# Optimization experiments

Hardware: AMD Instinct MI355X
Metric: run time of the kernel (lower is better)

## Reference

```python
import jax, jax.numpy as jnp
import numpy as np

NC, NP_, E = 100000, 50000, 500000
DC, DP = 256, 128
HID, OUT = 64, 64
H1, H2 = 2, 1
SLOPE = 0.2


def setup_inputs() -> dict:
    key = jax.random.key(0)
    ks = jax.random.split(key, 32)
    d = {}
    d['x_customer'] = jax.random.normal(ks[0], (NC, DC), jnp.float32)
    d['x_product'] = jax.random.normal(ks[1], (NP_, DP), jnp.float32)
    d['edge_src'] = jax.random.randint(ks[2], (E,), 0, NC, jnp.int32)
    d['edge_dst'] = jax.random.randint(ks[3], (E,), 0, NP_, jnp.int32)
    s = 0.1
    # layer1, edge type (customer, buys, product): src=customer, dst=product
    d['w1b_src'] = jax.random.normal(ks[4], (DC, H1 * HID)) * s
    d['w1b_dst'] = jax.random.normal(ks[5], (DP, H1 * HID)) * s
    d['a1b_src'] = jax.random.normal(ks[6], (H1, HID)) * s
    d['a1b_dst'] = jax.random.normal(ks[7], (H1, HID)) * s
    d['b1b'] = jnp.zeros((H1 * HID,), jnp.float32)
    # layer1, edge type (product, rev_buys, customer): src=product, dst=customer
    d['w1r_src'] = jax.random.normal(ks[8], (DP, H1 * HID)) * s
    d['w1r_dst'] = jax.random.normal(ks[9], (DC, H1 * HID)) * s
    d['a1r_src'] = jax.random.normal(ks[10], (H1, HID)) * s
    d['a1r_dst'] = jax.random.normal(ks[11], (H1, HID)) * s
    d['b1r'] = jnp.zeros((H1 * HID,), jnp.float32)
    # layer2 (input dim = H1*HID = 128 for both node types), heads=1
    d['w2b_src'] = jax.random.normal(ks[12], (H1 * HID, H2 * OUT)) * s
    d['w2b_dst'] = jax.random.normal(ks[13], (H1 * HID, H2 * OUT)) * s
    d['a2b_src'] = jax.random.normal(ks[14], (H2, OUT)) * s
    d['a2b_dst'] = jax.random.normal(ks[15], (H2, OUT)) * s
    d['b2b'] = jnp.zeros((H2 * OUT,), jnp.float32)
    d['w2r_src'] = jax.random.normal(ks[16], (H1 * HID, H2 * OUT)) * s
    d['w2r_dst'] = jax.random.normal(ks[17], (H1 * HID, H2 * OUT)) * s
    d['a2r_src'] = jax.random.normal(ks[18], (H2, OUT)) * s
    d['a2r_dst'] = jax.random.normal(ks[19], (H2, OUT)) * s
    d['b2r'] = jnp.zeros((H2 * OUT,), jnp.float32)
    return d


def _gat_conv(h_src, h_dst, e_src, e_dst, att_src, att_dst, bias, n_dst):
    # h_src: [Ns,H,C] projected source feats; h_dst: [Nd,H,C]
    a_s = (h_src * att_src).sum(-1)  # [Ns,H]
    a_d = (h_dst * att_dst).sum(-1)  # [Nd,H]
    alpha = jax.nn.leaky_relu(a_s[e_src] + a_d[e_dst], negative_slope=SLOPE)  # [E,H]
    m = jax.lax.stop_gradient(jax.ops.segment_max(alpha, e_dst, num_segments=n_dst))
    ex = jnp.exp(alpha - m[e_dst])
    den = jax.ops.segment_sum(ex, e_dst, num_segments=n_dst)
    w = ex / (den[e_dst] + 1e-16)  # segment softmax over incoming edges
    msg = h_src[e_src] * w[..., None]  # [E,H,C]
    out = jax.ops.segment_sum(msg, e_dst, num_segments=n_dst)  # [Nd,H,C]
    return out.reshape(n_dst, -1) + bias


def reference(x_customer, x_product, edge_src, edge_dst,
              w1b_src, w1b_dst, a1b_src, a1b_dst, b1b,
              w1r_src, w1r_dst, a1r_src, a1r_dst, b1r,
              w2b_src, w2b_dst, a2b_src, a2b_dst, b2b,
              w2r_src, w2r_dst, a2r_src, a2r_dst, b2r):
    # ---- layer 1 (heads=2, concat) ----
    hs = (x_customer @ w1b_src).reshape(NC, H1, HID)
    hd = (x_product @ w1b_dst).reshape(NP_, H1, HID)
    p1 = _gat_conv(hs, hd, edge_src, edge_dst, a1b_src, a1b_dst, b1b, NP_)
    hs = (x_product @ w1r_src).reshape(NP_, H1, HID)
    hd = (x_customer @ w1r_dst).reshape(NC, H1, HID)
    c1 = _gat_conv(hs, hd, edge_dst, edge_src, a1r_src, a1r_dst, b1r, NC)
    c1 = jax.nn.relu(c1)
    p1 = jax.nn.relu(p1)
    # ---- layer 2 (heads=1) ----
    hs = (c1 @ w2b_src).reshape(NC, H2, OUT)
    hd = (p1 @ w2b_dst).reshape(NP_, H2, OUT)
    p2 = _gat_conv(hs, hd, edge_src, edge_dst, a2b_src, a2b_dst, b2b, NP_)
    hs = (p1 @ w2r_src).reshape(NP_, H2, OUT)
    hd = (c1 @ w2r_dst).reshape(NC, H2, OUT)
    c2 = _gat_conv(hs, hd, edge_dst, edge_src, a2r_src, a2r_dst, b2r, NC)
    return c2, p2
```

## Files before the change

### kernel.cpp

```cpp
#include <hip/hip_runtime.h>
#include <hip/hip_bf16.h>

typedef __bf16 bf16_t;
typedef bf16_t bf16x2 __attribute__((ext_vector_type(2)));
typedef bf16_t bf16x4 __attribute__((ext_vector_type(4)));
typedef bf16_t bf16x8 __attribute__((ext_vector_type(8)));
typedef float f32x2 __attribute__((ext_vector_type(2)));
typedef float f32x4 __attribute__((ext_vector_type(4)));

static constexpr int NCn = 100000;
static constexpr int NPn = 50000;
static constexpr int NE  = 500000;

__device__ __forceinline__ float ldin(const void* p, size_t i, int fp32) {
    return fp32 ? ((const float*)p)[i] : (float)((const bf16_t*)p)[i];
}

__global__ __launch_bounds__(64) void detect_dtype(const void* x, int* flag) {
    const bf16_t* xb = (const bf16_t*)x;
    int lane = threadIdx.x;
    int bad = 0;
    for (int i = lane; i < 512; i += 64) {
        float v = (float)xb[i];
        if (!(v > -1e4f && v < 1e4f)) bad = 1;
    }
    unsigned long long m = __ballot(bad);
    if (lane == 0) flag[0] = (m != 0ull) ? 1 : 0;
}

__global__ __launch_bounds__(256) void zero_int(int* __restrict__ p, int n) {
    int i = blockIdx.x * 256 + threadIdx.x;
    if (i < n) p[i] = 0;
}
__global__ __launch_bounds__(256) void copy_int(const int* __restrict__ s,
                                                int* __restrict__ d, int n) {
    int i = blockIdx.x * 256 + threadIdx.x;
    if (i < n) d[i] = s[i];
}

__global__ __launch_bounds__(256) void prep_V(const int* __restrict__ flag,
                                              const void* w1bd, const void* a1bd,
                                              const void* w1rd, const void* a1rd,
                                              const void* w2bd, const void* a2bd,
                                              const void* w2rd, const void* a2rd,
                                              float* V1bd, float* V1rd,
                                              float* V2bd, float* V2rd) {
    int fp32 = flag[0];
    int t = threadIdx.x;
    for (int idx = t; idx < 256; idx += 256) {
        int k = idx >> 1, h = idx & 1;
        float s = 0.f;
        for (int c = 0; c < 64; ++c)
            s += ldin(w1bd, (size_t)k * 128 + h * 64 + c, fp32) * ldin(a1bd, h * 64 + c, fp32);
        V1bd[k * 2 + h] = s;
    }
    for (int idx = t; idx < 512; idx += 256) {
        int k = idx >> 1, h = idx & 1;
        float s = 0.f;
        for (int c = 0; c < 64; ++c)
            s += ldin(w1rd, (size_t)k * 128 + h * 64 + c, fp32) * ldin(a1rd, h * 64 + c, fp32);
        V1rd[k * 2 + h] = s;
    }
    for (int k = t; k < 128; k += 256) {
        float s = 0.f;
        for (int c = 0; c < 64; ++c)
            s += ldin(w2bd, (size_t)k * 64 + c, fp32) * ldin(a2bd, c, fp32);
        V2bd[k] = s;
    }
    for (int k = t; k < 128; k += 256) {
        float s = 0.f;
        for (int c = 0; c < 64; ++c)
            s += ldin(w2rd, (size_t)k * 64 + c, fp32) * ldin(a2rd, c, fp32);
        V2rd[k] = s;
    }
}

__global__ __launch_bounds__(256) void prep_w(const void* __restrict__ W,
                                              bf16_t* __restrict__ Wt,
                                              int N, int ks,
                                              const int* __restrict__ flag) {
    int fp32 = flag[0];
    int idx = blockIdx.x * 256 + threadIdx.x;
    int K = 1 << ks;
    int n = idx >> ks, k = idx & (K - 1);
    if (n < N) Wt[idx] = (bf16_t)ldin(W, (size_t)k * N + n, fp32);
}

template<int K>
__global__ __launch_bounds__(256) void cvt_rows(const void* __restrict__ X,
                                                bf16_t* __restrict__ Xb,
                                                const float* __restrict__ V,
                                                float* __restrict__ ad,
                                                int M, const int* __restrict__ flag) {
    constexpr int EPL = K / 64;
    int fp32 = flag[0];
    int wid = (blockIdx.x * 256 + threadIdx.x) >> 6;
    int lane = threadIdx.x & 63;
    if (wid >= M) return;
    size_t base = (size_t)wid * K + lane * EPL;
    float x[EPL];
    if constexpr (EPL == 4) {
        if (fp32) { f32x4 t = *(const f32x4*)((const float*)X + base);
#pragma unroll
            for (int j = 0; j < 4; ++j) x[j] = t[j];
        } else { bf16x4 t = *(const bf16x4*)((const bf16_t*)X + base);
#pragma unroll
            for (int j = 0; j < 4; ++j) x[j] = (float)t[j];
        }
        bf16x4 o;
#pragma unroll
        for (int j = 0; j < 4; ++j) o[j] = (bf16_t)x[j];
        *(bf16x4*)(Xb + base) = o;
    } else {
        if (fp32) { f32x2 t = *(const f32x2*)((const float*)X + base);
#pragma unroll
            for (int j = 0; j < 2; ++j) x[j] = t[j];
        } else { bf16x2 t = *(const bf16x2*)((const bf16_t*)X + base);
#pragma unroll
            for (int j = 0; j < 2; ++j) x[j] = (float)t[j];
        }
        bf16x2 o;
#pragma unroll
        for (int j = 0; j < 2; ++j) o[j] = (bf16_t)x[j];
        *(bf16x2*)(Xb + base) = o;
    }
    float a0 = 0.f, a1 = 0.f;
#pragma unroll
    for (int j = 0; j < EPL; ++j) {
        int k = lane * EPL + j;
        a0 += x[j] * V[k * 2];
        a1 += x[j] * V[k * 2 + 1];
    }
    for (int off = 32; off; off >>= 1) {
        a0 += __shfl_down(a0, off);
        a1 += __shfl_down(a1, off);
    }
    if (lane == 0) { ad[(size_t)wid * 2] = a0; ad[(size_t)wid * 2 + 1] = a1; }
}

__global__ __launch_bounds__(256) void hist_k(const int* __restrict__ dst,
                                              int* __restrict__ cnt, int E) {
    int e = blockIdx.x * 256 + threadIdx.x;
    if (e < E) atomicAdd(&cnt[dst[e]], 1);
}

__global__ __launch_bounds__(256) void scan_blocks(const int* __restrict__ cnt,
                                                   int* __restrict__ rs,
                                                   int* __restrict__ bsum, int N) {
    int t = threadIdx.x, b = blockIdx.x;
    int base = b * 1024 + t * 4;
    int c[4];
#pragma unroll
    for (int k = 0; k < 4; ++k) { int i = base + k; c[k] = (i < N) ? cnt[i] : 0; }
    int tsum = c[0] + c[1] + c[2] + c[3];
    __shared__ int sd[256];
    sd[t] = tsum;
    __syncthreads();
    for (int off = 1; off < 256; off <<= 1) {
        int x = (t >= off) ? sd[t - off] : 0;
        __syncthreads();
        sd[t] += x;
        __syncthreads();
    }
    int run = sd[t] - tsum;
#pragma unroll
    for (int k = 0; k < 4; ++k) { int i = base + k; if (i < N) rs[i] = run; run += c[k]; }
    if (t == 255) bsum[b] = sd[255];
}

__global__ __launch_bounds__(128) void scan_bsum(int* bsum, int nb) {
    int t = threadIdx.x;
    __shared__ int sd[128];
    int v = (t < nb) ? bsum[t] : 0;
    sd[t] = v;
    __syncthreads();
    for (int off = 1; off < 128; off <<= 1) {
        int x = (t >= off) ? sd[t - off] : 0;
        __syncthreads();
        sd[t] += x;
        __syncthreads();
    }
    if (t < nb) bsum[t] = sd[t] - v;
}

__global__ __launch_bounds__(256) void scan_add(int* __restrict__ rs,
                                                const int* __restrict__ bsum,
                                                int N, int E) {
    int i = blockIdx.x * 256 + threadIdx.x;
    if (i < N) rs[i] += bsum[i >> 10];
    if (i == 0) rs[N] = E;
}

__global__ __launch_bounds__(256) void scatter_k(const int* __restrict__ dst,
                                                 const int* __restrict__ nbr,
                                                 int* __restrict__ cur,
                                                 int* __restrict__ srcs,
                                                 int* __restrict__ dsts, int E) {
    int e = blockIdx.x * 256 + threadIdx.x;
    if (e >= E) return;
    int d = dst[e];
    int pos = atomicAdd(&cur[d], 1);
    srcs[pos] = nbr[e];
    dsts[pos] = d;
}

template<int K>
__global__ __launch_bounds__(256) void gemm_nl(const bf16_t* __restrict__ A,
                                               const bf16_t* __restrict__ Wt,
                                               bf16_t* __restrict__ C,
                                               int M, int N) {
    const int w = threadIdx.x >> 6;
    const int lane = threadIdx.x & 63;
    const int lm = lane & 15;
    const int lq = lane >> 4;
    const int n0 = blockIdx.y * 64;
    const int r0 = blockIdx.x * 128 + w * 32;
    int ra0 = r0 + lm;       if (ra0 > M - 1) ra0 = M - 1;
    int ra1 = r0 + 16 + lm;  if (ra1 > M - 1) ra1 = M - 1;
    const bf16_t* A0 = A + (size_t)ra0 * K + lq * 8;
    const bf16_t* A1 = A + (size_t)ra1 * K + lq * 8;
    const bf16_t* B0 = Wt + (size_t)(n0 + lm) * K + lq * 8;
    f32x4 acc[2][4] = {};
#pragma unroll
    for (int kt = 0; kt < K / 32; ++kt) {
        bf16x8 a0 = *(const bf16x8*)(A0 + kt * 32);
        bf16x8 a1 = *(const bf16x8*)(A1 + kt * 32);
#pragma unroll
        for (int nt = 0; nt < 4; ++nt) {
            bf16x8 b = *(const bf16x8*)(B0 + (size_t)nt * 16 * K + kt * 32);
            acc[0][nt] = __builtin_amdgcn_mfma_f32_16x16x32_bf16(a0, b, acc[0][nt], 0, 0, 0);
            acc[1][nt] = __builtin_amdgcn_mfma_f32_16x16x32_bf16(a1, b, acc[1][nt], 0, 0, 0);
        }
    }
#pragma unroll
    for (int rt = 0; rt < 2; ++rt) {
        const int crow0 = r0 + rt * 16 + lq * 4;
#pragma unroll
        for (int nt = 0; nt < 4; ++nt) {
            int col = n0 + nt * 16 + lm;
#pragma unroll
            for (int i = 0; i < 4; ++i) {
                int r = crow0 + i;
                if (r < M) C[(size_t)r * N + col] = (bf16_t)acc[rt][nt][i];
            }
        }
    }
}

__global__ __launch_bounds__(256) void att_dot(const bf16_t* __restrict__ Hb,
                                               const void* __restrict__ att,
                                               float* __restrict__ out,
                                               int Nn, int HD, int H,
                                               const int* __restrict__ flag) {
    int fp32 = flag[0];
    int wid = (blockIdx.x * 256 + threadIdx.x) >> 6;
    int lane = threadIdx.x & 63;
    if (wid >= Nn) return;
    const bf16_t* hp = Hb + (size_t)wid * HD;
    float p0 = (float)hp[lane] * ldin(att, lane, fp32);
    float p1 = 0.f;
    if (HD > 64) p1 = (float)hp[64 + lane] * ldin(att, 64 + lane, fp32);
    for (int off = 32; off; off >>= 1) {
        p0 += __shfl_down(p0, off);
        p1 += __shfl_down(p1, off);
    }
    if (lane == 0) {
        out[(size_t)wid * H] = p0;
        if (H == 2) out[(size_t)wid * H + 1] = p1;
    }
}

template<int H>
__global__ __launch_bounds__(256) void edge_ex(const int* __restrict__ srcs,
                                               const int* __restrict__ dsts,
                                               const float* __restrict__ as_,
                                               const float* __restrict__ ad_,
                                               float* __restrict__ ex, int E) {
    int i = blockIdx.x * 256 + threadIdx.x;
    if (i >= E) return;
    int s = srcs[i], d = dsts[i];
    if constexpr (H == 2) {
        f32x2 a = *(const f32x2*)(as_ + 2 * (size_t)s);
        f32x2 b = *(const f32x2*)(ad_ + 2 * (size_t)d);
        float v0 = a[0] + b[0]; v0 = v0 > 0.f ? v0 : 0.2f * v0;
        float v1 = a[1] + b[1]; v1 = v1 > 0.f ? v1 : 0.2f * v1;
        f32x2 o;
        o[0] = __expf(fminf(v0, 60.f));
        o[1] = __expf(fminf(v1, 60.f));
        *(f32x2*)(ex + 2 * (size_t)i) = o;
    } else {
        float v = as_[s] + ad_[d];
        v = v > 0.f ? v : 0.2f * v;
        ex[i] = __expf(fminf(v, 60.f));
    }
}

template<int HD, int MODE>
__global__ __launch_bounds__(256) void aggregate(const int* __restrict__ rs,
                                                 const int* __restrict__ srcs,
                                                 const float* __restrict__ ex,
                                                 const bf16_t* __restrict__ Hm,
                                                 const void* __restrict__ bias,
                                                 void* __restrict__ outb, size_t obase,
                                                 const float* __restrict__ V2,
                                                 float* __restrict__ ad2,
                                                 int Nd, const int* __restrict__ flag) {
    constexpr int NH = HD / 64;
    int wid = (blockIdx.x * 256 + threadIdx.x) >> 6;
    int lane = threadIdx.x & 63;
    if (wid >= Nd) return;
    int start = rs[wid], end = rs[wid + 1];
    int fp32 = flag[0];
    const int hsel = lane >> 5;

    float den = 0.f, acc0 = 0.f, acc1 = 0.f;
#pragma unroll 4
    for (int j = start; j < end; ++j) {
        int s = srcs[j];
        if constexpr (NH == 2) {
            f32x2 e = *(const f32x2*)(ex + 2 * (size_t)j);
            float eh = hsel ? e[1] : e[0];
            den += eh;
            bf16x2 hv = *(const bf16x2*)(Hm + (size_t)s * 128 + 2 * lane);
            acc0 += (float)hv[0] * eh;
            acc1 += (float)hv[1] * eh;
        } else {
            float eh = ex[j];
            den += eh;
            acc0 += (float)Hm[(size_t)s * 64 + lane] * eh;
        }
    }
    float inv = 1.f / (den + 1e-16f);

    if constexpr (MODE == 0) {
        int c0 = 2 * lane;
        float o0 = fmaxf(acc0 * inv + ldin(bias, c0, fp32), 0.f);
        float o1 = fmaxf(acc1 * inv + ldin(bias, c0 + 1, fp32), 0.f);
        bf16x2 ov;
        ov[0] = (bf16_t)o0;
        ov[1] = (bf16_t)o1;
        *(bf16x2*)((bf16_t*)outb + (size_t)wid * 128 + c0) = ov;
        float pp = o0 * V2[c0] + o1 * V2[c0 + 1];
        for (int off = 32; off; off >>= 1) pp += __shfl_down(pp, off);
        if (lane == 0) ad2[wid] = pp;
    } else {
        float o = acc0 * inv + ldin(bias, lane, fp32);
        size_t oi = obase + (size_t)wid * 64 + lane;
        if (fp32) ((float*)outb)[oi] = o;
        else      ((bf16_t*)outb)[oi] = (bf16_t)o;
    }
}

extern "C" void kernel_launch(void* const* d_in, const int* in_sizes, int n_in,
                              void* d_out, int out_size, void* d_ws, size_t ws_size,
                              hipStream_t stream) {
    const void* xc = d_in[0];
    const void* xp = d_in[1];
    const int* esrc = (const int*)d_in[2];
    const int* edst = (const int*)d_in[3];
    const void* w1b_src = d_in[4];
    const void* w1b_dst = d_in[5];
    const void* a1b_src = d_in[6];
    const void* a1b_dst = d_in[7];
    const void* b1b     = d_in[8];
    const void* w1r_src = d_in[9];
    const void* w1r_dst = d_in[10];
    const void* a1r_src = d_in[11];
    const void* a1r_dst = d_in[12];
    const void* b1r     = d_in[13];
    const void* w2b_src = d_in[14];
    const void* w2b_dst = d_in[15];
    const void* a2b_src = d_in[16];
    const void* a2b_dst = d_in[17];
    const void* b2b     = d_in[18];
    const void* w2r_src = d_in[19];
    const void* w2r_dst = d_in[20];
    const void* a2r_src = d_in[21];
    const void* a2r_dst = d_in[22];
    const void* b2r     = d_in[23];

    char* p = (char*)d_ws;
    auto alloc = [&](size_t nbytes) {
        char* r = p;
        p += (nbytes + 255) & ~(size_t)255;
        return r;
    };
    int* flag   = (int*)alloc(256);
    float* V1bd = (float*)alloc(256 * 4);
    float* V1rd = (float*)alloc(512 * 4);
    float* V2bd = (float*)alloc(128 * 4);
    float* V2rd = (float*)alloc(128 * 4);
    bf16_t* Wt1b = (bf16_t*)alloc(128 * 256 * 2);
    bf16_t* Wt1r = (bf16_t*)alloc(128 * 128 * 2);
    bf16_t* Wt2b = (bf16_t*)alloc(64 * 128 * 2);
    bf16_t* Wt2r = (bf16_t*)alloc(64 * 128 * 2);
    float* as_s = (float*)alloc((size_t)NCn * 2 * 4);
    float* ad_b = (float*)alloc((size_t)NPn * 2 * 4);
    float* ad_r = (float*)alloc((size_t)NCn * 2 * 4);
    float* ad2_b = (float*)alloc((size_t)NPn * 4);
    float* ad2_r = (float*)alloc((size_t)NCn * 4);
    int* rsB    = (int*)alloc((size_t)(NPn + 1) * 4);
    int* rsR    = (int*)alloc((size_t)(NCn + 1) * 4);
    int* srcsB  = (int*)alloc((size_t)NE * 4);
    int* srcsR  = (int*)alloc((size_t)NE * 4);
    int* dstsB  = (int*)alloc((size_t)NE * 4);
    int* dstsR  = (int*)alloc((size_t)NE * 4);
    float* exB  = (float*)alloc((size_t)NE * 2 * 4);
    float* exR  = (float*)alloc((size_t)NE * 2 * 4);
    int* cntB   = (int*)alloc((size_t)NPn * 4);
    int* cntR   = (int*)alloc((size_t)NCn * 4);
    int* bsum   = (int*)alloc(128 * 4);
    bf16_t* xcb = (bf16_t*)alloc((size_t)NCn * 256 * 2);
    bf16_t* xpb = (bf16_t*)alloc((size_t)NPn * 128 * 2);
    bf16_t* Hc  = (bf16_t*)alloc((size_t)NCn * 128 * 2);
    bf16_t* Hp  = (bf16_t*)alloc((size_t)NPn * 128 * 2);
    bf16_t* c1  = (bf16_t*)alloc((size_t)NCn * 128 * 2);
    bf16_t* p1  = (bf16_t*)alloc((size_t)NPn * 128 * 2);
    bf16_t* Hc2 = (bf16_t*)alloc((size_t)NCn * 64 * 2);
    bf16_t* Hp2 = (bf16_t*)alloc((size_t)NPn * 64 * 2);

    const dim3 blk(256);
    const int gE = (NE + 255) / 256;
    const int sbP = (NPn + 1023) / 1024;
    const int sbR = (NCn + 1023) / 1024;
    const int gmC = (NCn + 127) / 128;
    const int gmP = (NPn + 127) / 128;
    const int gNP = (NPn + 255) / 256;
    const int gNC = (NCn + 255) / 256;

    detect_dtype<<<1, 64, 0, stream>>>(xc, flag);
    prep_V<<<1, 256, 0, stream>>>(flag, w1b_dst, a1b_dst, w1r_dst, a1r_dst,
                                  w2b_dst, a2b_dst, w2r_dst, a2r_dst,
                                  V1bd, V1rd, V2bd, V2rd);
    prep_w<<<128, blk, 0, stream>>>(w1b_src, Wt1b, 128, 8, flag);
    prep_w<<<64,  blk, 0, stream>>>(w1r_src, Wt1r, 128, 7, flag);
    prep_w<<<32,  blk, 0, stream>>>(w2b_src, Wt2b, 64, 7, flag);
    prep_w<<<32,  blk, 0, stream>>>(w2r_src, Wt2r, 64, 7, flag);

    zero_int<<<gNP, blk, 0, stream>>>(cntB, NPn);
    hist_k<<<gE, blk, 0, stream>>>(edst, cntB, NE);
    scan_blocks<<<sbP, blk, 0, stream>>>(cntB, rsB, bsum, NPn);
    scan_bsum<<<1, 128, 0, stream>>>(bsum, sbP);
    scan_add<<<gNP + 1, blk, 0, stream>>>(rsB, bsum, NPn, NE);
    copy_int<<<gNP, blk, 0, stream>>>(rsB, cntB, NPn);
    scatter_k<<<gE, blk, 0, stream>>>(edst, esrc, cntB, srcsB, dstsB, NE);

    zero_int<<<gNC, blk, 0, stream>>>(cntR, NCn);
    hist_k<<<gE, blk, 0, stream>>>(esrc, cntR, NE);
    scan_blocks<<<sbR, blk, 0, stream>>>(cntR, rsR, bsum, NCn);
    scan_bsum<<<1, 128, 0, stream>>>(bsum, sbR);
    scan_add<<<gNC + 1, blk, 0, stream>>>(rsR, bsum, NCn, NE);
    copy_int<<<gNC, blk, 0, stream>>>(rsR, cntR, NCn);
    scatter_k<<<gE, blk, 0, stream>>>(esrc, edst, cntR, srcsR, dstsR, NE);

    cvt_rows<256><<<(NCn + 3) / 4, blk, 0, stream>>>(xc, xcb, V1rd, ad_r, NCn, flag);
    cvt_rows<128><<<(NPn + 3) / 4, blk, 0, stream>>>(xp, xpb, V1bd, ad_b, NPn, flag);

    gemm_nl<256><<<dim3(gmC, 2), blk, 0, stream>>>(xcb, Wt1b, Hc, NCn, 128);
    gemm_nl<128><<<dim3(gmP, 2), blk, 0, stream>>>(xpb, Wt1r, Hp, NPn, 128);

    att_dot<<<(NCn + 3) / 4, blk, 0, stream>>>(Hc, a1b_src, as_s, NCn, 128, 2, flag);
    edge_ex<2><<<gE, blk, 0, stream>>>(srcsB, dstsB, as_s, ad_b, exB, NE);
    aggregate<128, 0><<<(NPn + 3) / 4, blk, 0, stream>>>(rsB, srcsB, exB, Hc, b1b, p1, 0, V2bd, ad2_b, NPn, flag);

    att_dot<<<(NPn + 3) / 4, blk, 0, stream>>>(Hp, a1r_src, as_s, NPn, 128, 2, flag);
    edge_ex<2><<<gE, blk, 0, stream>>>(srcsR, dstsR, as_s, ad_r, exR, NE);
    aggregate<128, 0><<<(NCn + 3) / 4, blk, 0, stream>>>(rsR, srcsR, exR, Hp, b1r, c1, 0, V2rd, ad2_r, NCn, flag);

    gemm_nl<128><<<dim3(gmC, 1), blk, 0, stream>>>(c1, Wt2b, Hc2, NCn, 64);
    gemm_nl<128><<<dim3(gmP, 1), blk, 0, stream>>>(p1, Wt2r, Hp2, NPn, 64);

    att_dot<<<(NCn + 3) / 4, blk, 0, stream>>>(Hc2, a2b_src, as_s, NCn, 64, 1, flag);
    edge_ex<1><<<gE, blk, 0, stream>>>(srcsB, dstsB, as_s, ad2_b, exB, NE);
    aggregate<64, 1><<<(NPn + 3) / 4, blk, 0, stream>>>(rsB, srcsB, exB, Hc2, b2b, d_out, (size_t)NCn * 64, nullptr, nullptr, NPn, flag);

    att_dot<<<(NPn + 3) / 4, blk, 0, stream>>>(Hp2, a2r_src, as_s, NPn, 64, 1, flag);
    edge_ex<1><<<gE, blk, 0, stream>>>(srcsR, dstsR, as_s, ad2_r, exR, NE);
    aggregate<64, 1><<<(NCn + 3) / 4, blk, 0, stream>>>(rsR, srcsR, exR, Hp2, b2r, d_out, 0, nullptr, nullptr, NCn, flag);
}
```

Baseline: 717.3 us.

## Fuse attention dot into GEMM epilogue and merge per-edge-type kernels

```diff
diff --git a/kernel.cpp b/kernel.cpp
--- a/kernel.cpp
+++ b/kernel.cpp
@@ -16,37 +16,27 @@
     return fp32 ? ((const float*)p)[i] : (float)((const bf16_t*)p)[i];
 }
 
-__global__ __launch_bounds__(64) void detect_dtype(const void* x, int* flag) {
-    const bf16_t* xb = (const bf16_t*)x;
-    int lane = threadIdx.x;
-    int bad = 0;
-    for (int i = lane; i < 512; i += 64) {
-        float v = (float)xb[i];
-        if (!(v > -1e4f && v < 1e4f)) bad = 1;
-    }
-    unsigned long long m = __ballot(bad);
-    if (lane == 0) flag[0] = (m != 0ull) ? 1 : 0;
-}
-
-__global__ __launch_bounds__(256) void zero_int(int* __restrict__ p, int n) {
-    int i = blockIdx.x * 256 + threadIdx.x;
-    if (i < n) p[i] = 0;
-}
-__global__ __launch_bounds__(256) void copy_int(const int* __restrict__ s,
-                                                int* __restrict__ d, int n) {
-    int i = blockIdx.x * 256 + threadIdx.x;
-    if (i < n) d[i] = s[i];
-}
-
-__global__ __launch_bounds__(256) void prep_V(const int* __restrict__ flag,
-                                              const void* w1bd, const void* a1bd,
-                                              const void* w1rd, const void* a1rd,
-                                              const void* w2bd, const void* a2bd,
-                                              const void* w2rd, const void* a2rd,
-                                              float* V1bd, float* V1rd,
-                                              float* V2bd, float* V2rd) {
-    int fp32 = flag[0];
+__global__ __launch_bounds__(256) void prep_meta(const void* x, int* flag,
+                                                 const void* w1bd, const void* a1bd,
+                                                 const void* w1rd, const void* a1rd,
+                                                 const void* w2bd, const void* a2bd,
+                                                 const void* w2rd, const void* a2rd,
+                                                 float* V1bd, float* V1rd,
+                                                 float* V2bd, float* V2rd) {
+    __shared__ int sflag;
     int t = threadIdx.x;
+    if (t < 64) {
+        const bf16_t* xb = (const bf16_t*)x;
+        int bad = 0;
+        for (int i = t; i < 512; i += 64) {
+            float v = (float)xb[i];
+            if (!(v > -1e4f && v < 1e4f)) bad = 1;
+        }
+        unsigned long long m = __ballot(bad);
+        if (t == 0) { sflag = (m != 0ull) ? 1 : 0; flag[0] = sflag; }
+    }
+    __syncthreads();
+    int fp32 = sflag;
     for (int idx = t; idx < 256; idx += 256) {
         int k = idx >> 1, h = idx & 1;
         float s = 0.f;
@@ -75,12 +65,19 @@
     }
 }
 
-__global__ __launch_bounds__(256) void prep_w(const void* __restrict__ W,
-                                              bf16_t* __restrict__ Wt,
-                                              int N, int ks,
-                                              const int* __restrict__ flag) {
+__global__ __launch_bounds__(256) void prep_w4(const void* __restrict__ w1b, bf16_t* __restrict__ Wt1b,
+                                               const void* __restrict__ w1r, bf16_t* __restrict__ Wt1r,
+                                               const void* __restrict__ w2b, bf16_t* __restrict__ Wt2b,
+                                               const void* __restrict__ w2r, bf16_t* __restrict__ Wt2r,
+                                               const int* __restrict__ flag) {
     int fp32 = flag[0];
-    int idx = blockIdx.x * 256 + threadIdx.x;
+    int b = blockIdx.x;
+    const void* W; bf16_t* Wt; int N, ks, base;
+    if (b < 128)      { W = w1b; Wt = Wt1b; N = 128; ks = 8; base = 0;   }
+    else if (b < 192) { W = w1r; Wt = Wt1r; N = 128; ks = 7; base = 128; }
+    else if (b < 224) { W = w2b; Wt = Wt2b; N = 64;  ks = 7; base = 192; }
+    else              { W = w2r; Wt = Wt2r; N = 64;  ks = 7; base = 224; }
+    int idx = (b - base) * 256 + threadIdx.x;
     int K = 1 << ks;
     int n = idx >> ks, k = idx & (K - 1);
     if (n < N) Wt[idx] = (bf16_t)ldin(W, (size_t)k * N + n, fp32);
@@ -138,10 +135,21 @@
     if (lane == 0) { ad[(size_t)wid * 2] = a0; ad[(size_t)wid * 2 + 1] = a1; }
 }
 
-__global__ __launch_bounds__(256) void hist_k(const int* __restrict__ dst,
-                                              int* __restrict__ cnt, int E) {
+__global__ __launch_bounds__(256) void zero2(int* __restrict__ a, int na,
+                                             int* __restrict__ b, int nb) {
+    int i = blockIdx.x * 256 + threadIdx.x;
+    if (i < na) a[i] = 0;
+    else if (i - na < nb) b[i - na] = 0;
+}
+
+__global__ __launch_bounds__(256) void hist2(const int* __restrict__ esrc,
+                                             const int* __restrict__ edst,
+                                             int* __restrict__ cntR,
+                                             int* __restrict__ cntB, int E) {
     int e = blockIdx.x * 256 + threadIdx.x;
-    if (e < E) atomicAdd(&cnt[dst[e]], 1);
+    if (e >= E) return;
+    atomicAdd(&cntB[edst[e]], 1);
+    atomicAdd(&cntR[esrc[e]], 1);
 }
 
 __global__ __launch_bounds__(256) void scan_blocks(const int* __restrict__ cnt,
@@ -168,7 +176,10 @@
     if (t == 255) bsum[b] = sd[255];
 }
 
-__global__ __launch_bounds__(128) void scan_bsum(int* bsum, int nb) {
+__global__ __launch_bounds__(128) void scan_bsum2(int* __restrict__ bsumB, int nbB,
+                                                  int* __restrict__ bsumR, int nbR) {
+    int* bsum = blockIdx.x ? bsumR : bsumB;
+    int nb = blockIdx.x ? nbR : nbB;
     int t = threadIdx.x;
     __shared__ int sd[128];
     int v = (t < nb) ? bsum[t] : 0;
@@ -183,32 +194,39 @@
     if (t < nb) bsum[t] = sd[t] - v;
 }
 
-__global__ __launch_bounds__(256) void scan_add(int* __restrict__ rs,
-                                                const int* __restrict__ bsum,
-                                                int N, int E) {
+__global__ __launch_bounds__(256) void scan_add2(int* __restrict__ rsB, const int* __restrict__ bsumB,
+                                                 int NB, int* __restrict__ cntB,
+                                                 int* __restrict__ rsR, const int* __restrict__ bsumR,
+                                                 int NR, int* __restrict__ cntR, int E) {
     int i = blockIdx.x * 256 + threadIdx.x;
-    if (i < N) rs[i] += bsum[i >> 10];
-    if (i == 0) rs[N] = E;
-}
-
-__global__ __launch_bounds__(256) void scatter_k(const int* __restrict__ dst,
-                                                 const int* __restrict__ nbr,
-                                                 int* __restrict__ cur,
-                                                 int* __restrict__ srcs,
-                                                 int* __restrict__ dsts, int E) {
+    if (i < NB) { int v = rsB[i] + bsumB[i >> 10]; rsB[i] = v; cntB[i] = v; }
+    if (i < NR) { int v = rsR[i] + bsumR[i >> 10]; rsR[i] = v; cntR[i] = v; }
+    if (i == 0) { rsB[NB] = E; rsR[NR] = E; }
+}
+
+__global__ __launch_bounds__(256) void scatter2(const int* __restrict__ esrc,
+                                                const int* __restrict__ edst,
+                                                int* __restrict__ curB, int* __restrict__ curR,
+                                                int* __restrict__ srcsB, int* __restrict__ dstsB,
+                                                int* __restrict__ srcsR, int* __restrict__ dstsR,
+                                                int E) {
     int e = blockIdx.x * 256 + threadIdx.x;
     if (e >= E) return;
-    int d = dst[e];
-    int pos = atomicAdd(&cur[d], 1);
-    srcs[pos] = nbr[e];
-    dsts[pos] = d;
+    int s = esrc[e], d = edst[e];
+    int pb = atomicAdd(&curB[d], 1);
+    srcsB[pb] = s; dstsB[pb] = d;
+    int pr = atomicAdd(&curR[s], 1);
+    srcsR[pr] = d; dstsR[pr] = s;
 }
 
 template<int K>
 __global__ __launch_bounds__(256) void gemm_nl(const bf16_t* __restrict__ A,
                                                const bf16_t* __restrict__ Wt,
                                                bf16_t* __restrict__ C,
-                                               int M, int N) {
+                                               const void* __restrict__ att,
+                                               float* __restrict__ asout, int H,
+                                               int M, int N,
+                                               const int* __restrict__ flag) {
     const int w = threadIdx.x >> 6;
     const int lane = threadIdx.x & 63;
     const int lm = lane & 15;
@@ -245,40 +263,58 @@
             }
         }
     }
-}
-
-__global__ __launch_bounds__(256) void att_dot(const bf16_t* __restrict__ Hb,
-                                               const void* __restrict__ att,
-                                               float* __restrict__ out,
-                                               int Nn, int HD, int H,
-                                               const int* __restrict__ flag) {
     int fp32 = flag[0];
-    int wid = (blockIdx.x * 256 + threadIdx.x) >> 6;
-    int lane = threadIdx.x & 63;
-    if (wid >= Nn) return;
-    const bf16_t* hp = Hb + (size_t)wid * HD;
-    float p0 = (float)hp[lane] * ldin(att, lane, fp32);
-    float p1 = 0.f;
-    if (HD > 64) p1 = (float)hp[64 + lane] * ldin(att, 64 + lane, fp32);
-    for (int off = 32; off; off >>= 1) {
-        p0 += __shfl_down(p0, off);
-        p1 += __shfl_down(p1, off);
-    }
-    if (lane == 0) {
-        out[(size_t)wid * H] = p0;
-        if (H == 2) out[(size_t)wid * H + 1] = p1;
+    float attv[4];
+#pragma unroll
+    for (int nt = 0; nt < 4; ++nt) attv[nt] = ldin(att, n0 + nt * 16 + lm, fp32);
+    float part[2][4];
+#pragma unroll
+    for (int rt = 0; rt < 2; ++rt)
+#pragma unroll
+        for (int i = 0; i < 4; ++i) {
+            float s = 0.f;
+#pragma unroll
+            for (int nt = 0; nt < 4; ++nt) s += acc[rt][nt][i] * attv[nt];
+            part[rt][i] = s;
+        }
+#pragma unroll
+    for (int off = 1; off < 16; off <<= 1)
+#pragma unroll
+        for (int rt = 0; rt < 2; ++rt)
+#pragma unroll
+            for (int i = 0; i < 4; ++i)
+                part[rt][i] += __shfl_xor(part[rt][i], off);
+    if (lm == 0) {
+#pragma unroll
+        for (int rt = 0; rt < 2; ++rt)
+#pragma unroll
+            for (int i = 0; i < 4; ++i) {
+                int r = r0 + rt * 16 + lq * 4 + i;
+                if (r < M) asout[(size_t)r * H + blockIdx.y] = part[rt][i];
+            }
     }
 }
 
 template<int H>
-__global__ __launch_bounds__(256) void edge_ex(const int* __restrict__ srcs,
-                                               const int* __restrict__ dsts,
-                                               const float* __restrict__ as_,
-                                               const float* __restrict__ ad_,
-                                               float* __restrict__ ex, int E) {
+__global__ __launch_bounds__(256) void edge_ex2(const int* __restrict__ srcsB,
+                                                const int* __restrict__ dstsB,
+                                                const float* __restrict__ asB,
+                                                const float* __restrict__ adB,
+                                                float* __restrict__ exBp,
+                                                const int* __restrict__ srcsR,
+                                                const int* __restrict__ dstsR,
+                                                const float* __restrict__ asR,
+                                                const float* __restrict__ adR,
+                                                float* __restrict__ exRp, int E) {
     int i = blockIdx.x * 256 + threadIdx.x;
-    if (i >= E) return;
-    int s = srcs[i], d = dsts[i];
+    const int *srcs, *dsts; const float *as_, *ad_; float* ex; int j;
+    if (i < E) { j = i; srcs = srcsB; dsts = dstsB; as_ = asB; ad_ = adB; ex = exBp; }
+    else {
+        j = i - E;
+        if (j >= E) return;
+        srcs = srcsR; dsts = dstsR; as_ = asR; ad_ = adR; ex = exRp;
+    }
+    int s = srcs[j], d = dsts[j];
     if constexpr (H == 2) {
         f32x2 a = *(const f32x2*)(as_ + 2 * (size_t)s);
         f32x2 b = *(const f32x2*)(ad_ + 2 * (size_t)d);
@@ -287,28 +323,40 @@
         f32x2 o;
         o[0] = __expf(fminf(v0, 60.f));
         o[1] = __expf(fminf(v1, 60.f));
-        *(f32x2*)(ex + 2 * (size_t)i) = o;
+        *(f32x2*)(ex + 2 * (size_t)j) = o;
     } else {
         float v = as_[s] + ad_[d];
         v = v > 0.f ? v : 0.2f * v;
-        ex[i] = __expf(fminf(v, 60.f));
+        ex[j] = __expf(fminf(v, 60.f));
     }
 }
 
 template<int HD, int MODE>
-__global__ __launch_bounds__(256) void aggregate(const int* __restrict__ rs,
-                                                 const int* __restrict__ srcs,
-                                                 const float* __restrict__ ex,
-                                                 const bf16_t* __restrict__ Hm,
-                                                 const void* __restrict__ bias,
-                                                 void* __restrict__ outb, size_t obase,
-                                                 const float* __restrict__ V2,
-                                                 float* __restrict__ ad2,
-                                                 int Nd, const int* __restrict__ flag) {
+__global__ __launch_bounds__(256) void aggregate2(
+        const int* __restrict__ rsB, const int* __restrict__ srcsB,
+        const float* __restrict__ exB, const bf16_t* __restrict__ HmB,
+        const void* __restrict__ biasB, const float* __restrict__ V2B,
+        float* __restrict__ ad2B, void* __restrict__ outB, size_t obaseB, int NdB,
+        const int* __restrict__ rsR, const int* __restrict__ srcsR,
+        const float* __restrict__ exR, const bf16_t* __restrict__ HmR,
+        const void* __restrict__ biasR, const float* __restrict__ V2R,
+        float* __restrict__ ad2R, void* __restrict__ outR, size_t obaseR, int NdR,
+        const int* __restrict__ flag) {
     constexpr int NH = HD / 64;
-    int wid = (blockIdx.x * 256 + threadIdx.x) >> 6;
+    int gw = (blockIdx.x * 256 + threadIdx.x) >> 6;
     int lane = threadIdx.x & 63;
-    if (wid >= Nd) return;
+    const int* rs; const int* srcs; const float* ex; const bf16_t* Hm;
+    const void* bias; const float* V2; float* ad2; void* outb; size_t obase; int wid;
+    if (gw < NdB) {
+        wid = gw;
+        rs = rsB; srcs = srcsB; ex = exB; Hm = HmB; bias = biasB;
+        V2 = V2B; ad2 = ad2B; outb = outB; obase = obaseB;
+    } else {
+        wid = gw - NdB;
+        if (wid >= NdR) return;
+        rs = rsR; srcs = srcsR; ex = exR; Hm = HmR; bias = biasR;
+        V2 = V2R; ad2 = ad2R; outb = outR; obase = obaseR;
+    }
     int start = rs[wid], end = rs[wid + 1];
     int fp32 = flag[0];
     const int hsel = lane >> 5;
@@ -394,7 +442,10 @@
     bf16_t* Wt1r = (bf16_t*)alloc(128 * 128 * 2);
     bf16_t* Wt2b = (bf16_t*)alloc(64 * 128 * 2);
     bf16_t* Wt2r = (bf16_t*)alloc(64 * 128 * 2);
-    float* as_s = (float*)alloc((size_t)NCn * 2 * 4);
+    float* as_b = (float*)alloc((size_t)NCn * 2 * 4);
+    float* as_r = (float*)alloc((size_t)NPn * 2 * 4);
+    float* as2_c = (float*)alloc((size_t)NCn * 4);
+    float* as2_p = (float*)alloc((size_t)NPn * 4);
     float* ad_b = (float*)alloc((size_t)NPn * 2 * 4);
     float* ad_r = (float*)alloc((size_t)NCn * 2 * 4);
     float* ad2_b = (float*)alloc((size_t)NPn * 4);
@@ -409,7 +460,8 @@
     float* exR  = (float*)alloc((size_t)NE * 2 * 4);
     int* cntB   = (int*)alloc((size_t)NPn * 4);
     int* cntR   = (int*)alloc((size_t)NCn * 4);
-    int* bsum   = (int*)alloc(128 * 4);
+    int* bsumB  = (int*)alloc(128 * 4);
+    int* bsumR  = (int*)alloc(128 * 4);
     bf16_t* xcb = (bf16_t*)alloc((size_t)NCn * 256 * 2);
     bf16_t* xpb = (bf16_t*)alloc((size_t)NPn * 128 * 2);
     bf16_t* Hc  = (bf16_t*)alloc((size_t)NCn * 128 * 2);
@@ -421,60 +473,47 @@
 
     const dim3 blk(256);
     const int gE = (NE + 255) / 256;
+    const int g2E = (2 * NE + 255) / 256;
     const int sbP = (NPn + 1023) / 1024;
     const int sbR = (NCn + 1023) / 1024;
     const int gmC = (NCn + 127) / 128;
     const int gmP = (NPn + 127) / 128;
-    const int gNP = (NPn + 255) / 256;
     const int gNC = (NCn + 255) / 256;
-
-    detect_dtype<<<1, 64, 0, stream>>>(xc, flag);
-    prep_V<<<1, 256, 0, stream>>>(flag, w1b_dst, a1b_dst, w1r_dst, a1r_dst,
-                                  w2b_dst, a2b_dst, w2r_dst, a2r_dst,
-                                  V1bd, V1rd, V2bd, V2rd);
-    prep_w<<<128, blk, 0, stream>>>(w1b_src, Wt1b, 128, 8, flag);
-    prep_w<<<64,  blk, 0, stream>>>(w1r_src, Wt1r, 128, 7, flag);
-    prep_w<<<32,  blk, 0, stream>>>(w2b_src, Wt2b, 64, 7, flag);
-    prep_w<<<32,  blk, 0, stream>>>(w2r_src, Wt2r, 64, 7, flag);
-
-    zero_int<<<gNP, blk, 0, stream>>>(cntB, NPn);
-    hist_k<<<gE, blk, 0, stream>>>(edst, cntB, NE);
-    scan_blocks<<<sbP, blk, 0, stream>>>(cntB, rsB, bsum, NPn);
-    scan_bsum<<<1, 128, 0, stream>>>(bsum, sbP);
-    scan_add<<<gNP + 1, blk, 0, stream>>>(rsB, bsum, NPn, NE);
-    copy_int<<<gNP, blk, 0, stream>>>(rsB, cntB, NPn);
-    scatter_k<<<gE, blk, 0, stream>>>(edst, esrc, cntB, srcsB, dstsB, NE);
-
-    zero_int<<<gNC, blk, 0, stream>>>(cntR, NCn);
-    hist_k<<<gE, blk, 0, stream>>>(esrc, cntR, NE);
-    scan_blocks<<<sbR, blk, 0, stream>>>(cntR, rsR, bsum, NCn);
-    scan_bsum<<<1, 128, 0, stream>>>(bsum, sbR);
-    scan_add<<<gNC + 1, blk, 0, stream>>>(rsR, bsum, NCn, NE);
-    copy_int<<<gNC, blk, 0, stream>>>(rsR, cntR, NCn);
-    scatter_k<<<gE, blk, 0, stream>>>(esrc, edst, cntR, srcsR, dstsR, NE);
+    const int gBoth = (NPn + NCn + 255) / 256;
+    const int gAgg = (NPn + NCn + 3) / 4;
+
+    prep_meta<<<1, 256, 0, stream>>>(xc, flag, w1b_dst, a1b_dst, w1r_dst, a1r_dst,
+                                     w2b_dst, a2b_dst, w2r_dst, a2r_dst,
+                                     V1bd, V1rd, V2bd, V2rd);
+    prep_w4<<<256, blk, 0, stream>>>(w1b_src, Wt1b, w1r_src, Wt1r,
+                                     w2b_src, Wt2b, w2r_src, Wt2r, flag);
+
+    zero2<<<gBoth, blk, 0, stream>>>(cntB, NPn, cntR, NCn);
+    hist2<<<gE, blk, 0, stream>>>(esrc, edst, cntR, cntB, NE);
+    scan_blocks<<<sbP, blk, 0, stream>>>(cntB, rsB, bsumB, NPn);
+    scan_blocks<<<sbR, blk, 0, stream>>>(cntR, rsR, bsumR, NCn);
+    scan_bsum2<<<2, 128, 0, stream>>>(bsumB, sbP, bsumR, sbR);
+    scan_add2<<<gNC, blk, 0, stream>>>(rsB, bsumB, NPn, cntB, rsR, bsumR, NCn, cntR, NE);
+    scatter2<<<gE, blk, 0, stream>>>(esrc, edst, cntB, cntR, srcsB, dstsB, srcsR, dstsR, NE);
 
     cvt_rows<256><<<(NCn + 3) / 4, blk, 0, stream>>>(xc, xcb, V1rd, ad_r, NCn, flag);
     cvt_rows<128><<<(NPn + 3) / 4, blk, 0, stream>>>(xp, xpb, V1bd, ad_b, NPn, flag);
 
-    gemm_nl<256><<<dim3(gmC, 2), blk, 0, stream>>>(xcb, Wt1b, Hc, NCn, 128);
-    gemm_nl<128><<<dim3(gmP, 2), blk, 0, stream>>>(xpb, Wt1r, Hp, NPn, 128);
-
-    att_dot<<<(NCn + 3) / 4, blk, 0, stream>>>(Hc, a1b_src, as_s, NCn, 128, 2, flag);
-    edge_ex<2><<<gE, blk, 0, stream>>>(srcsB, dstsB, as_s, ad_b, exB, NE);
-    aggregate<128, 0><<<(NPn + 3) / 4, blk, 0, stream>>>(rsB, srcsB, exB, Hc, b1b, p1, 0, V2bd, ad2_b, NPn, flag);
-
-    att_dot<<<(NPn + 3) / 4, blk, 0, stream>>>(Hp, a1r_src, as_s, NPn, 128, 2, flag);
-    edge_ex<2><<<gE, blk, 0, stream>>>(srcsR, dstsR, as_s, ad_r, exR, NE);
-    aggregate<128, 0><<<(NCn + 3) / 4, blk, 0, stream>>>(rsR, srcsR, exR, Hp, b1r, c1, 0, V2rd, ad2_r, NCn, flag);
-
-    gemm_nl<128><<<dim3(gmC, 1), blk, 0, stream>>>(c1, Wt2b, Hc2, NCn, 64);
-    gemm_nl<128><<<dim3(gmP, 1), blk, 0, stream>>>(p1, Wt2r, Hp2, NPn, 64);
-
-    att_dot<<<(NCn + 3) / 4, blk, 0, stream>>>(Hc2, a2b_src, as_s, NCn, 64, 1, flag);
-    edge_ex<1><<<gE, blk, 0, stream>>>(srcsB, dstsB, as_s, ad2_b, exB, NE);
-    aggregate<64, 1><<<(NPn + 3) / 4, blk, 0, stream>>>(rsB, srcsB, exB, Hc2, b2b, d_out, (size_t)NCn * 64, nullptr, nullptr, NPn, flag);
-
-    att_dot<<<(NPn + 3) / 4, blk, 0, stream>>>(Hp2, a2r_src, as_s, NPn, 64, 1, flag);
-    edge_ex<1><<<gE, blk, 0, stream>>>(srcsR, dstsR, as_s, ad2_r, exR, NE);
-    aggregate<64, 1><<<(NCn + 3) / 4, blk, 0, stream>>>(rsR, srcsR, exR, Hp2, b2r, d_out, 0, nullptr, nullptr, NCn, flag);
-}
+    gemm_nl<256><<<dim3(gmC, 2), blk, 0, stream>>>(xcb, Wt1b, Hc, a1b_src, as_b, 2, NCn, 128, flag);
+    gemm_nl<128><<<dim3(gmP, 2), blk, 0, stream>>>(xpb, Wt1r, Hp, a1r_src, as_r, 2, NPn, 128, flag);
+
+    edge_ex2<2><<<g2E, blk, 0, stream>>>(srcsB, dstsB, as_b, ad_b, exB,
+                                         srcsR, dstsR, as_r, ad_r, exR, NE);
+    aggregate2<128, 0><<<gAgg, blk, 0, stream>>>(
+        rsB, srcsB, exB, Hc, b1b, V2bd, ad2_b, p1, 0, NPn,
+        rsR, srcsR, exR, Hp, b1r, V2rd, ad2_r, c1, 0, NCn, flag);
+
+    gemm_nl<128><<<dim3(gmC, 1), blk, 0, stream>>>(c1, Wt2b, Hc2, a2b_src, as2_c, 1, NCn, 64, flag);
+    gemm_nl<128><<<dim3(gmP, 1), blk, 0, stream>>>(p1, Wt2r, Hp2, a2r_src, as2_p, 1, NPn, 64, flag);
+
+    edge_ex2<1><<<g2E, blk, 0, stream>>>(srcsB, dstsB, as2_c, ad2_b, exB,
+                                         srcsR, dstsR, as2_p, ad2_r, exR, NE);
+    aggregate2<64, 1><<<gAgg, blk, 0, stream>>>(
+        rsB, srcsB, exB, Hc2, b2b, nullptr, nullptr, d_out, (size_t)NCn * 64, NPn,
+        rsR, srcsR, exR, Hp2, b2r, nullptr, nullptr, d_out, 0, NCn, flag);
+}
```

After: 622.9 us. -13.2%, faster.
